# Performance work log

Hardware: AMD Instinct MI355X
Metric: run time of the kernel (lower is better)

Reference implementation:

```python
import jax, jax.numpy as jnp
import numpy as np

N, E, G = 50000, 1600000, 8
IN, H, C = 64, 4, 32
HID = H * C  # 128
L = 3


def setup_inputs() -> dict:
    key = jax.random.key(0)
    ks = jax.random.split(key, 20)
    x = jax.random.normal(ks[0], (N, IN), dtype=jnp.float32)
    edge_index = jax.random.randint(ks[1], (2, E), 0, N, dtype=jnp.int64)
    batch = jnp.sort(jax.random.randint(ks[2], (N,), 0, G, dtype=jnp.int64))
    s = 0.05
    Wp = jax.random.normal(ks[3], (IN, HID), dtype=jnp.float32) * s
    bp = jnp.zeros((HID,), dtype=jnp.float32)
    Wl = jax.random.normal(ks[4], (L, HID, HID), dtype=jnp.float32) * s
    att_src = jax.random.normal(ks[5], (L, H, C), dtype=jnp.float32) * s
    att_dst = jax.random.normal(ks[6], (L, H, C), dtype=jnp.float32) * s
    bconv = jnp.zeros((L, HID), dtype=jnp.float32)
    W1 = jax.random.normal(ks[7], (2 * HID, 256), dtype=jnp.float32) * s
    b1 = jnp.zeros((256,), dtype=jnp.float32)
    W2 = jax.random.normal(ks[8], (256, 128), dtype=jnp.float32) * s
    b2 = jnp.zeros((128,), dtype=jnp.float32)
    W3 = jax.random.normal(ks[9], (128, 1), dtype=jnp.float32) * s
    b3 = jnp.zeros((1,), dtype=jnp.float32)
    return dict(x=x, edge_index=edge_index, batch=batch, Wp=Wp, bp=bp, Wl=Wl,
                att_src=att_src, att_dst=att_dst, bconv=bconv,
                W1=W1, b1=b1, W2=W2, b2=b2, W3=W3, b3=b3)


def _gat_layer(x, src, dst, W, a_src, a_dst, b):
    # PyG GATConv (concat=True, add_self_loops handled by caller via src/dst)
    h = (x @ W).reshape(N, H, C)                      # [N,H,C]
    asrc = jnp.sum(h * a_src, axis=-1)                # [N,H]
    adst = jnp.sum(h * a_dst, axis=-1)                # [N,H]
    e = jax.nn.leaky_relu(asrc[src] + adst[dst], 0.2)  # [E',H]
    m = jax.ops.segment_max(e, dst, num_segments=N)   # scatter-softmax over dst
    e = jnp.exp(e - m[dst])
    z = jax.ops.segment_sum(e, dst, num_segments=N)
    alpha = e / (z[dst] + 1e-16)                      # [E',H]
    out = jax.ops.segment_sum(h[src] * alpha[:, :, None], dst, num_segments=N)
    return out.reshape(N, HID) + b


def reference(x, edge_index, batch, Wp, bp, Wl, att_src, att_dst, bconv,
              W1, b1, W2, b2, W3, b3):
    # add self loops once (PyG default add_self_loops=True)
    loop = jnp.arange(N, dtype=edge_index.dtype)
    src = jnp.concatenate([edge_index[0], loop])
    dst = jnp.concatenate([edge_index[1], loop])

    h = jax.nn.relu(x @ Wp + bp)
    for l in range(L):
        h = jax.nn.relu(_gat_layer(h, src, dst, Wl[l], att_src[l], att_dst[l], bconv[l]))

    cnt = jax.ops.segment_sum(jnp.ones((N,), h.dtype), batch, num_segments=G)
    mean = jax.ops.segment_sum(h, batch, num_segments=G) / jnp.maximum(cnt, 1.0)[:, None]
    mx = jax.ops.segment_max(h, batch, num_segments=G)
    mx = jnp.where(cnt[:, None] > 0, mx, 0.0)
    p = jnp.concatenate([mean, mx], axis=-1)          # [G, 2*HID]

    p = jax.nn.relu(p @ W1 + b1)
    p = jax.nn.relu(p @ W2 + b2)
    return (p @ W3 + b3).squeeze(-1)                  # [G]
```

## Files before the change

### kernel.cpp

```cpp
#include <hip/hip_runtime.h>
#include <math.h>

#define NN 50000
#define GG 8
#define HEADS 4
#define CH 32
#define HID 128
#define NLAYER 3
#define POOL_S 64
#define DEG_CAP 96
#define NBG2 ((NN + 63) / 64)
#define NBS 1024

__device__ float g_h[(size_t)NN * HID];
__device__ __attribute__((aligned(16))) unsigned short g_h2b[(size_t)NN * HID];
__device__ float g_as[(size_t)NN * HEADS];
__device__ float g_ad[(size_t)NN * HEADS];
__device__ int g_cursor[NN];
__device__ __attribute__((aligned(16))) unsigned short g_csr16[(size_t)NN * DEG_CAP];
__device__ int g_starts[GG + 1];
__device__ double g_psum[(size_t)GG * POOL_S * HID];
__device__ float g_pmax[(size_t)GG * POOL_S * HID];

__device__ __forceinline__ float lrelu(float v) { return v > 0.f ? v : 0.2f * v; }

__device__ __forceinline__ float bf2f(unsigned short u) {
    union { unsigned int i; float f; } v;
    v.i = ((unsigned int)u) << 16;
    return v.f;
}
__device__ __forceinline__ unsigned short f2bf(float f) {
    union { float f; unsigned int i; } v;
    v.f = f;
    unsigned int r = v.i + 0x7FFFu + ((v.i >> 16) & 1u);
    return (unsigned short)(r >> 16);
}

__global__ void zero_kernel() {
    int i = blockIdx.x * blockDim.x + threadIdx.x;
    if (i < NN) g_cursor[i] = 0;
}

template <int K, bool ATT, bool RELU, bool SRC_PARAM>
__device__ __forceinline__ void gemm_body(
    const float* __restrict__ Xp, const float* __restrict__ W, const float* __restrict__ bias,
    const float* __restrict__ att_s, const float* __restrict__ att_d, int n, int blk) {
    constexpr int KT = 32;
    constexpr int XS = 68;
    __shared__ float Ws[KT * 128];
    __shared__ float Xs[KT * XS];
    const float* X = SRC_PARAM ? Xp : g_h;
    int tid = threadIdx.x;
    int base = blk * 64;
    int rows = n - base;
    if (rows > 64) rows = 64;
    int cg = tid & 15, rg = tid >> 4;
    int c0 = cg * 8, r0 = rg * 4;
    float acc[4][8];
#pragma unroll
    for (int i = 0; i < 4; i++)
#pragma unroll
        for (int j = 0; j < 8; j++) acc[i][j] = 0.f;

    for (int kb = 0; kb < K; kb += KT) {
        {
            const float4* Wg = (const float4*)(W + (size_t)kb * 128);
            float4* Ws4 = (float4*)Ws;
#pragma unroll
            for (int u = 0; u < 4; u++) Ws4[tid + u * 256] = Wg[tid + u * 256];
        }
#pragma unroll
        for (int u = 0; u < 2; u++) {
            int i = tid + u * 256;
            int r = i >> 3, k4 = i & 7;
            float4 v = {0.f, 0.f, 0.f, 0.f};
            if (r < rows) v = *(const float4*)(X + (size_t)(base + r) * K + kb + k4 * 4);
            Xs[(k4 * 4 + 0) * XS + r] = v.x;
            Xs[(k4 * 4 + 1) * XS + r] = v.y;
            Xs[(k4 * 4 + 2) * XS + r] = v.z;
            Xs[(k4 * 4 + 3) * XS + r] = v.w;
        }
        __syncthreads();
#pragma unroll 8
        for (int k = 0; k < KT; k++) {
            const float4 xa = *(const float4*)&Xs[k * XS + r0];
            const float4 wa = *(const float4*)&Ws[k * 128 + c0];
            const float4 wb = *(const float4*)&Ws[k * 128 + c0 + 4];
            const float xr[4] = {xa.x, xa.y, xa.z, xa.w};
            const float wr[8] = {wa.x, wa.y, wa.z, wa.w, wb.x, wb.y, wb.z, wb.w};
#pragma unroll
            for (int ii = 0; ii < 4; ii++)
#pragma unroll
                for (int jj = 0; jj < 8; jj++) acc[ii][jj] += xr[ii] * wr[jj];
        }
        __syncthreads();
    }

    if constexpr (!ATT) {
        float bv[8];
#pragma unroll
        for (int j = 0; j < 8; j++) bv[j] = bias ? bias[c0 + j] : 0.f;
#pragma unroll
        for (int ii = 0; ii < 4; ii++) {
            int r = r0 + ii;
            if (r < rows) {
                float o[8];
#pragma unroll
                for (int jj = 0; jj < 8; jj++) {
                    o[jj] = acc[ii][jj] + bv[jj];
                    if (RELU) o[jj] = fmaxf(o[jj], 0.f);
                }
                float4 oa = {o[0], o[1], o[2], o[3]};
                float4 ob = {o[4], o[5], o[6], o[7]};
                *(float4*)&g_h[(size_t)(base + r) * 128 + c0] = oa;
                *(float4*)&g_h[(size_t)(base + r) * 128 + c0 + 4] = ob;
            }
        }
    } else {
#pragma unroll
        for (int ii = 0; ii < 4; ii++) {
            int r = r0 + ii;
            if (r < rows) {
                uint4 pk;
                pk.x = (unsigned)f2bf(acc[ii][0]) | ((unsigned)f2bf(acc[ii][1]) << 16);
                pk.y = (unsigned)f2bf(acc[ii][2]) | ((unsigned)f2bf(acc[ii][3]) << 16);
                pk.z = (unsigned)f2bf(acc[ii][4]) | ((unsigned)f2bf(acc[ii][5]) << 16);
                pk.w = (unsigned)f2bf(acc[ii][6]) | ((unsigned)f2bf(acc[ii][7]) << 16);
                *(uint4*)&g_h2b[(size_t)(base + r) * 128 + c0] = pk;
            }
        }
        float avs[8], avd[8];
#pragma unroll
        for (int j = 0; j < 8; j++) { avs[j] = att_s[c0 + j]; avd[j] = att_d[c0 + j]; }
#pragma unroll
        for (int ii = 0; ii < 4; ii++) {
            float ps = 0.f, pd = 0.f;
#pragma unroll
            for (int jj = 0; jj < 8; jj++) { ps += acc[ii][jj] * avs[jj]; pd += acc[ii][jj] * avd[jj]; }
            ps += __shfl_xor(ps, 1); ps += __shfl_xor(ps, 2);
            pd += __shfl_xor(pd, 1); pd += __shfl_xor(pd, 2);
            int r = r0 + ii;
            if ((cg & 3) == 0 && r < rows) {
                g_as[(size_t)(base + r) * 4 + (cg >> 2)] = ps;
                g_ad[(size_t)(base + r) * 4 + (cg >> 2)] = pd;
            }
        }
    }
}

template <int K, bool ATT, bool RELU, bool SRC_PARAM>
__global__ __launch_bounds__(256) void gemm_kernel(
    const float* __restrict__ Xp, const float* __restrict__ W, const float* __restrict__ bias,
    const float* __restrict__ att_s, const float* __restrict__ att_d, int n) {
    gemm_body<K, ATT, RELU, SRC_PARAM>(Xp, W, bias, att_s, att_d, n, blockIdx.x);
}

template <int K, bool ATT, bool RELU, bool SRC_PARAM>
__global__ __launch_bounds__(256) void fat_kernel(
    const float* __restrict__ Xp, const float* __restrict__ W, const float* __restrict__ bias,
    const float* __restrict__ as_, const float* __restrict__ ad_,
    const int* __restrict__ srcv, const int* __restrict__ dstv, int ebeg, int eend) {
    if (blockIdx.x < NBG2) {
        gemm_body<K, ATT, RELU, SRC_PARAM>(Xp, W, bias, as_, ad_, NN, blockIdx.x);
    } else {
        int idx = ebeg + (blockIdx.x - NBG2) * 256 + threadIdx.x;
        int stride = (gridDim.x - NBG2) * 256;
        for (int j = idx; j < eend; j += stride) {
            int d = dstv[j];
            int pos = atomicAdd(&g_cursor[d], 1);
            if (pos < DEG_CAP) g_csr16[(size_t)d * DEG_CAP + pos] = (unsigned short)srcv[j];
        }
    }
}

__global__ __launch_bounds__(256) void gat_layer_kernel(const float* __restrict__ bconv) {
    int wave = threadIdx.x >> 6;
    int lane = threadIdx.x & 63;
    int i = blockIdx.x * 4 + wave;

    int deg = g_cursor[i];
    if (deg > DEG_CAP) deg = DEG_CAP;

    int stream = lane >> 5;
    int sl = lane & 31;
    int hl = sl >> 3;
    int li = sl & 7;
    int c0 = sl * 4;
    int bsel = lane & 56;

    float ad_h = g_ad[(size_t)i * 4 + hl];
    const unsigned short* csr = &g_csr16[(size_t)i * DEG_CAP];

    float4 acc = {0.f, 0.f, 0.f, 0.f};
    float zraw = 0.f;

    int nfull = deg >> 4;
    for (int t = 0; t < nfull; ++t) {
        int j0 = t * 16 + stream * 8;
        uint4 cs = *(const uint4*)(csr + j0);
        int s0 = cs.x & 0xFFFF, s1 = cs.x >> 16;
        int s2 = cs.y & 0xFFFF, s3 = cs.y >> 16;
        int s4 = cs.z & 0xFFFF, s5 = cs.z >> 16;
        int s6 = cs.w & 0xFFFF, s7 = cs.w >> 16;
        ushort4 q0 = *(const ushort4*)&g_h2b[(s0 << 7) + c0];
        ushort4 q1 = *(const ushort4*)&g_h2b[(s1 << 7) + c0];
        ushort4 q2 = *(const ushort4*)&g_h2b[(s2 << 7) + c0];
        ushort4 q3 = *(const ushort4*)&g_h2b[(s3 << 7) + c0];
        ushort4 q4 = *(const ushort4*)&g_h2b[(s4 << 7) + c0];
        ushort4 q5 = *(const ushort4*)&g_h2b[(s5 << 7) + c0];
        ushort4 q6 = *(const ushort4*)&g_h2b[(s6 << 7) + c0];
        ushort4 q7 = *(const ushort4*)&g_h2b[(s7 << 7) + c0];
        unsigned wsel = li < 4 ? (li < 2 ? cs.x : cs.y) : (li < 6 ? cs.z : cs.w);
        int sm = (li & 1) ? (int)(wsel >> 16) : (int)(wsel & 0xFFFF);
        float a = g_as[(sm << 2) + hl];
        float wr = expf(lrelu(a + ad_h));
        zraw += wr;
        float w0 = __shfl(wr, bsel | 0);
        float w1 = __shfl(wr, bsel | 1);
        float w2 = __shfl(wr, bsel | 2);
        float w3 = __shfl(wr, bsel | 3);
        float w4 = __shfl(wr, bsel | 4);
        float w5 = __shfl(wr, bsel | 5);
        float w6 = __shfl(wr, bsel | 6);
        float w7 = __shfl(wr, bsel | 7);
        acc.x += w0 * bf2f(q0.x); acc.y += w0 * bf2f(q0.y); acc.z += w0 * bf2f(q0.z); acc.w += w0 * bf2f(q0.w);
        acc.x += w1 * bf2f(q1.x); acc.y += w1 * bf2f(q1.y); acc.z += w1 * bf2f(q1.z); acc.w += w1 * bf2f(q1.w);
        acc.x += w2 * bf2f(q2.x); acc.y += w2 * bf2f(q2.y); acc.z += w2 * bf2f(q2.z); acc.w += w2 * bf2f(q2.w);
        acc.x += w3 * bf2f(q3.x); acc.y += w3 * bf2f(q3.y); acc.z += w3 * bf2f(q3.z); acc.w += w3 * bf2f(q3.w);
        acc.x += w4 * bf2f(q4.x); acc.y += w4 * bf2f(q4.y); acc.z += w4 * bf2f(q4.z); acc.w += w4 * bf2f(q4.w);
        acc.x += w5 * bf2f(q5.x); acc.y += w5 * bf2f(q5.y); acc.z += w5 * bf2f(q5.z); acc.w += w5 * bf2f(q5.w);
        acc.x += w6 * bf2f(q6.x); acc.y += w6 * bf2f(q6.y); acc.z += w6 * bf2f(q6.z); acc.w += w6 * bf2f(q6.w);
        acc.x += w7 * bf2f(q7.x); acc.y += w7 * bf2f(q7.y); acc.z += w7 * bf2f(q7.z); acc.w += w7 * bf2f(q7.w);
    }

    int tbase = nfull * 16 + stream * 8;
#pragma unroll
    for (int k = 0; k < 8; ++k) {
        if (tbase + k < deg) {
            int s = csr[tbase + k];
            float a = g_as[(s << 2) + hl];
            float wr = expf(lrelu(a + ad_h));
            zraw += wr * 0.125f;
            ushort4 q = *(const ushort4*)&g_h2b[(s << 7) + c0];
            acc.x += wr * bf2f(q.x); acc.y += wr * bf2f(q.y);
            acc.z += wr * bf2f(q.z); acc.w += wr * bf2f(q.w);
        }
    }

    acc.x += __shfl_xor(acc.x, 32);
    acc.y += __shfl_xor(acc.y, 32);
    acc.z += __shfl_xor(acc.z, 32);
    acc.w += __shfl_xor(acc.w, 32);
    zraw += __shfl_xor(zraw, 1);
    zraw += __shfl_xor(zraw, 2);
    zraw += __shfl_xor(zraw, 4);
    zraw += __shfl_xor(zraw, 32);

    if (lane < 32) {
        float as_i = g_as[(i << 2) + hl];
        float sw = expf(lrelu(as_i + ad_h));
        float invz = 1.f / (zraw + sw + 1e-16f);
        ushort4 qs = *(const ushort4*)&g_h2b[(i << 7) + c0];
        float4 bc = *(const float4*)&bconv[c0];
        float4 o;
        o.x = fmaxf((sw * bf2f(qs.x) + acc.x) * invz + bc.x, 0.f);
        o.y = fmaxf((sw * bf2f(qs.y) + acc.y) * invz + bc.y, 0.f);
        o.z = fmaxf((sw * bf2f(qs.z) + acc.z) * invz + bc.z, 0.f);
        o.w = fmaxf((sw * bf2f(qs.w) + acc.w) * invz + bc.w, 0.f);
        *(float4*)&g_h[(size_t)i * 128 + c0] = o;
    }
}

__global__ void bounds_kernel(const int* __restrict__ batch) {
    int t = threadIdx.x;
    if (t > GG) return;
    int lo = 0, hi = NN;
    while (lo < hi) {
        int mid = (lo + hi) >> 1;
        if (batch[mid] < t) lo = mid + 1; else hi = mid;
    }
    g_starts[t] = lo;
}

__global__ void pool1_kernel() {
    int g = blockIdx.x / POOL_S, s = blockIdx.x % POOL_S;
    int n0 = g_starts[g], n1 = g_starts[g + 1];
    long long cnt = n1 - n0;
    int a = n0 + (int)(cnt * s / POOL_S);
    int b = n0 + (int)(cnt * (s + 1) / POOL_S);
    int c = threadIdx.x;
    double sum = 0.0;
    float mx = -INFINITY;
    for (int nn = a; nn < b; nn++) {
        float v = g_h[(size_t)nn * 128 + c];
        sum += v;
        mx = fmaxf(mx, v);
    }
    g_psum[(size_t)blockIdx.x * 128 + c] = sum;
    g_pmax[(size_t)blockIdx.x * 128 + c] = mx;
}

__global__ __launch_bounds__(256) void head_kernel(
    const float* __restrict__ W1, const float* __restrict__ b1,
    const float* __restrict__ W2, const float* __restrict__ b2,
    const float* __restrict__ W3, const float* __restrict__ b3,
    float* __restrict__ outv) {
    __shared__ float p[256];
    __shared__ float r1[256];
    __shared__ float r2[128];
    int g = blockIdx.x, t = threadIdx.x;
    int cnt = g_starts[g + 1] - g_starts[g];
    if (t < 128) {
        double s = 0.0;
        for (int q = 0; q < POOL_S; q++) s += g_psum[(size_t)(g * POOL_S + q) * 128 + t];
        double dcnt = cnt > 0 ? (double)cnt : 1.0;
        p[t] = (float)(s / dcnt);
    } else {
        int c = t - 128;
        float mx = -INFINITY;
        for (int q = 0; q < POOL_S; q++) mx = fmaxf(mx, g_pmax[(size_t)(g * POOL_S + q) * 128 + c]);
        p[t] = cnt > 0 ? mx : 0.f;
    }
    __syncthreads();
    float acc = b1[t];
    for (int k = 0; k < 256; k++) acc += p[k] * W1[k * 256 + t];
    r1[t] = fmaxf(acc, 0.f);
    __syncthreads();
    if (t < 128) {
        float a2 = b2[t];
        for (int k = 0; k < 256; k++) a2 += r1[k] * W2[k * 128 + t];
        r2[t] = fmaxf(a2, 0.f);
    }
    __syncthreads();
    if (t < 64) {
        float a3 = r2[t] * W3[t] + r2[t + 64] * W3[t + 64];
#pragma unroll
        for (int d = 32; d >= 1; d >>= 1) a3 += __shfl_down(a3, d);
        if (t == 0) outv[g] = a3 + b3[0];
    }
}

extern "C" void kernel_launch(void* const* d_in, const int* in_sizes, int n_in,
                              void* d_out, int out_size, void* d_ws, size_t ws_size,
                              hipStream_t stream) {
    const float* x = (const float*)d_in[0];
    const int* eidx = (const int*)d_in[1];
    const int* batch = (const int*)d_in[2];
    const float* Wp = (const float*)d_in[3];
    const float* bp = (const float*)d_in[4];
    const float* Wl = (const float*)d_in[5];
    const float* att_src = (const float*)d_in[6];
    const float* att_dst = (const float*)d_in[7];
    const float* bconv = (const float*)d_in[8];
    const float* W1 = (const float*)d_in[9];
    const float* b1 = (const float*)d_in[10];
    const float* W2 = (const float*)d_in[11];
    const float* b2 = (const float*)d_in[12];
    const float* W3 = (const float*)d_in[13];
    const float* b3 = (const float*)d_in[14];
    float* out = (float*)d_out;
    int E = in_sizes[1] / 2;
    int Emid = E / 2;

    zero_kernel<<<(NN + 255) / 256, 256, 0, stream>>>();

    fat_kernel<64, false, true, true><<<NBG2 + NBS, 256, 0, stream>>>(
        x, Wp, bp, nullptr, nullptr, eidx, eidx + E, 0, Emid);

    fat_kernel<128, true, false, false><<<NBG2 + NBS, 256, 0, stream>>>(
        nullptr, Wl, nullptr, att_src, att_dst, eidx, eidx + E, Emid, E);

    gat_layer_kernel<<<NN / 4, 256, 0, stream>>>(bconv);

    for (int l = 1; l < NLAYER; l++) {
        gemm_kernel<128, true, false, false><<<NBG2, 256, 0, stream>>>(
            nullptr, Wl + (size_t)l * HID * HID, nullptr,
            att_src + (size_t)l * HEADS * CH, att_dst + (size_t)l * HEADS * CH, NN);
        gat_layer_kernel<<<NN / 4, 256, 0, stream>>>(bconv + (size_t)l * HID);
    }

    bounds_kernel<<<1, 64, 0, stream>>>(batch);
    pool1_kernel<<<GG * POOL_S, 128, 0, stream>>>();
    head_kernel<<<GG, 256, 0, stream>>>(W1, b1, W2, b2, W3, b3, out);
}
```

Before: 533.4 us.

## Use split-bf16 MFMA for GAT layer projections with hi/lo activation storage

Replaces the FP32 FMA tiled GEMM for the per-layer 128x128 projection with MFMA 16x16x32 bf16 instructions. Activations and weights are each split into bf16 high and low parts, and three products are accumulated to keep close to FP32 accuracy. The producing kernels now write hi/lo bf16 activations instead of fp32, and a weight-transpose prep kernel is added. This trades FP32 ALU work for matrix-core work, but adds extra conversion work and the weight-prep launch, and the operands are loaded straight from global memory without LDS staging.

```diff
diff --git a/kernel.cpp b/kernel.cpp
--- a/kernel.cpp
+++ b/kernel.cpp
@@ -12,8 +12,15 @@
 #define NBG2 ((NN + 63) / 64)
 #define NBS 1024
 
+typedef __attribute__((ext_vector_type(8))) short bf16x8;
+typedef __attribute__((ext_vector_type(4))) float f32x4;
+
 __device__ float g_h[(size_t)NN * HID];
 __device__ __attribute__((aligned(16))) unsigned short g_h2b[(size_t)NN * HID];
+__device__ __attribute__((aligned(16))) unsigned short g_xhi[(size_t)NN * HID];
+__device__ __attribute__((aligned(16))) unsigned short g_xlo[(size_t)NN * HID];
+__device__ __attribute__((aligned(16))) unsigned short g_wthi[(size_t)NLAYER * HID * HID];
+__device__ __attribute__((aligned(16))) unsigned short g_wtlo[(size_t)NLAYER * HID * HID];
 __device__ float g_as[(size_t)NN * HEADS];
 __device__ float g_ad[(size_t)NN * HEADS];
 __device__ int g_cursor[NN];
@@ -41,18 +48,30 @@
     if (i < NN) g_cursor[i] = 0;
 }
 
-template <int K, bool ATT, bool RELU, bool SRC_PARAM>
-__device__ __forceinline__ void gemm_body(
+__global__ void wprep_kernel(const float* __restrict__ Wl) {
+    int idx = blockIdx.x * 256 + threadIdx.x;
+    if (idx >= NLAYER * HID * HID) return;
+    int lay = idx / (HID * HID);
+    int rem = idx - lay * HID * HID;
+    int n = rem >> 7, k = rem & 127;
+    float v = Wl[(size_t)lay * HID * HID + (size_t)k * HID + n];
+    unsigned short h = f2bf(v);
+    float r = v - bf2f(h);
+    g_wthi[idx] = h;
+    g_wtlo[idx] = f2bf(r);
+}
+
+template <int K>
+__device__ __forceinline__ void proj_body(
     const float* __restrict__ Xp, const float* __restrict__ W, const float* __restrict__ bias,
-    const float* __restrict__ att_s, const float* __restrict__ att_d, int n, int blk) {
+    int blk) {
     constexpr int KT = 32;
     constexpr int XS = 68;
     __shared__ float Ws[KT * 128];
     __shared__ float Xs[KT * XS];
-    const float* X = SRC_PARAM ? Xp : g_h;
     int tid = threadIdx.x;
     int base = blk * 64;
-    int rows = n - base;
+    int rows = NN - base;
     if (rows > 64) rows = 64;
     int cg = tid & 15, rg = tid >> 4;
     int c0 = cg * 8, r0 = rg * 4;
@@ -74,7 +93,7 @@
             int i = tid + u * 256;
             int r = i >> 3, k4 = i & 7;
             float4 v = {0.f, 0.f, 0.f, 0.f};
-            if (r < rows) v = *(const float4*)(X + (size_t)(base + r) * K + kb + k4 * 4);
+            if (r < rows) v = *(const float4*)(Xp + (size_t)(base + r) * K + kb + k4 * 4);
             Xs[(k4 * 4 + 0) * XS + r] = v.x;
             Xs[(k4 * 4 + 1) * XS + r] = v.y;
             Xs[(k4 * 4 + 2) * XS + r] = v.z;
@@ -96,83 +115,137 @@
         __syncthreads();
     }
 
-    if constexpr (!ATT) {
-        float bv[8];
-#pragma unroll
-        for (int j = 0; j < 8; j++) bv[j] = bias ? bias[c0 + j] : 0.f;
-#pragma unroll
-        for (int ii = 0; ii < 4; ii++) {
-            int r = r0 + ii;
-            if (r < rows) {
-                float o[8];
-#pragma unroll
-                for (int jj = 0; jj < 8; jj++) {
-                    o[jj] = acc[ii][jj] + bv[jj];
-                    if (RELU) o[jj] = fmaxf(o[jj], 0.f);
-                }
-                float4 oa = {o[0], o[1], o[2], o[3]};
-                float4 ob = {o[4], o[5], o[6], o[7]};
-                *(float4*)&g_h[(size_t)(base + r) * 128 + c0] = oa;
-                *(float4*)&g_h[(size_t)(base + r) * 128 + c0 + 4] = ob;
-            }
-        }
-    } else {
-#pragma unroll
-        for (int ii = 0; ii < 4; ii++) {
-            int r = r0 + ii;
-            if (r < rows) {
-                uint4 pk;
-                pk.x = (unsigned)f2bf(acc[ii][0]) | ((unsigned)f2bf(acc[ii][1]) << 16);
-                pk.y = (unsigned)f2bf(acc[ii][2]) | ((unsigned)f2bf(acc[ii][3]) << 16);
-                pk.z = (unsigned)f2bf(acc[ii][4]) | ((unsigned)f2bf(acc[ii][5]) << 16);
-                pk.w = (unsigned)f2bf(acc[ii][6]) | ((unsigned)f2bf(acc[ii][7]) << 16);
-                *(uint4*)&g_h2b[(size_t)(base + r) * 128 + c0] = pk;
-            }
-        }
-        float avs[8], avd[8];
-#pragma unroll
-        for (int j = 0; j < 8; j++) { avs[j] = att_s[c0 + j]; avd[j] = att_d[c0 + j]; }
-#pragma unroll
-        for (int ii = 0; ii < 4; ii++) {
-            float ps = 0.f, pd = 0.f;
-#pragma unroll
-            for (int jj = 0; jj < 8; jj++) { ps += acc[ii][jj] * avs[jj]; pd += acc[ii][jj] * avd[jj]; }
-            ps += __shfl_xor(ps, 1); ps += __shfl_xor(ps, 2);
-            pd += __shfl_xor(pd, 1); pd += __shfl_xor(pd, 2);
-            int r = r0 + ii;
-            if ((cg & 3) == 0 && r < rows) {
-                g_as[(size_t)(base + r) * 4 + (cg >> 2)] = ps;
-                g_ad[(size_t)(base + r) * 4 + (cg >> 2)] = pd;
-            }
-        }
-    }
-}
-
-template <int K, bool ATT, bool RELU, bool SRC_PARAM>
-__global__ __launch_bounds__(256) void gemm_kernel(
+    float bv[8];
+#pragma unroll
+    for (int j = 0; j < 8; j++) bv[j] = bias[c0 + j];
+#pragma unroll
+    for (int ii = 0; ii < 4; ii++) {
+        int r = r0 + ii;
+        if (r < rows) {
+            ushort4 h0, l0, h1, l1;
+            float o[8];
+#pragma unroll
+            for (int jj = 0; jj < 8; jj++) o[jj] = fmaxf(acc[ii][jj] + bv[jj], 0.f);
+            h0.x = f2bf(o[0]); h0.y = f2bf(o[1]); h0.z = f2bf(o[2]); h0.w = f2bf(o[3]);
+            h1.x = f2bf(o[4]); h1.y = f2bf(o[5]); h1.z = f2bf(o[6]); h1.w = f2bf(o[7]);
+            l0.x = f2bf(o[0] - bf2f(h0.x)); l0.y = f2bf(o[1] - bf2f(h0.y));
+            l0.z = f2bf(o[2] - bf2f(h0.z)); l0.w = f2bf(o[3] - bf2f(h0.w));
+            l1.x = f2bf(o[4] - bf2f(h1.x)); l1.y = f2bf(o[5] - bf2f(h1.y));
+            l1.z = f2bf(o[6] - bf2f(h1.z)); l1.w = f2bf(o[7] - bf2f(h1.w));
+            size_t off = (size_t)(base + r) * 128 + c0;
+            *(ushort4*)&g_xhi[off] = h0;
+            *(ushort4*)&g_xhi[off + 4] = h1;
+            *(ushort4*)&g_xlo[off] = l0;
+            *(ushort4*)&g_xlo[off + 4] = l1;
+        }
+    }
+}
+
+__device__ __forceinline__ void mfma_att_body(
+    const float* __restrict__ att_s, const float* __restrict__ att_d,
+    int lay, int blk) {
+    __shared__ float Ysh[64][HID];
+    int tid = threadIdx.x;
+    int w = tid >> 6, l = tid & 63;
+    int base = blk * 64;
+    int rows = NN - base;
+    if (rows > 64) rows = 64;
+    int ar = l & 15, kg = l >> 4;
+    int arow = base + w * 16 + ar;
+    if (arow >= NN) arow = NN - 1;
+    const unsigned short* xh = g_xhi + (size_t)arow * HID + kg * 8;
+    const unsigned short* xl = g_xlo + (size_t)arow * HID + kg * 8;
+    const unsigned short* wh = g_wthi + (size_t)lay * HID * HID + (size_t)ar * HID + kg * 8;
+    const unsigned short* wl = g_wtlo + (size_t)lay * HID * HID + (size_t)ar * HID + kg * 8;
+
+    f32x4 acc[8];
+#pragma unroll
+    for (int ct = 0; ct < 8; ct++) acc[ct] = (f32x4){0.f, 0.f, 0.f, 0.f};
+
+#pragma unroll
+    for (int ks = 0; ks < 4; ks++) {
+        bf16x8 ah = *(const bf16x8*)(xh + ks * 32);
+        bf16x8 al = *(const bf16x8*)(xl + ks * 32);
+#pragma unroll
+        for (int ct = 0; ct < 8; ct++) {
+            bf16x8 bh = *(const bf16x8*)(wh + ct * 16 * HID + ks * 32);
+            bf16x8 bl = *(const bf16x8*)(wl + ct * 16 * HID + ks * 32);
+            acc[ct] = __builtin_amdgcn_mfma_f32_16x16x32_bf16(ah, bh, acc[ct], 0, 0, 0);
+            acc[ct] = __builtin_amdgcn_mfma_f32_16x16x32_bf16(al, bh, acc[ct], 0, 0, 0);
+            acc[ct] = __builtin_amdgcn_mfma_f32_16x16x32_bf16(ah, bl, acc[ct], 0, 0, 0);
+        }
+    }
+
+#pragma unroll
+    for (int ct = 0; ct < 8; ct++)
+#pragma unroll
+        for (int j = 0; j < 4; j++)
+            Ysh[w * 16 + kg * 4 + j][ct * 16 + ar] = acc[ct][j];
+    __syncthreads();
+
+    int cg = tid & 15, rg = tid >> 4;
+    int c0 = cg * 8, r0 = rg * 4;
+    float avs[8], avd[8];
+#pragma unroll
+    for (int j = 0; j < 8; j++) { avs[j] = att_s[c0 + j]; avd[j] = att_d[c0 + j]; }
+#pragma unroll
+    for (int ii = 0; ii < 4; ii++) {
+        int r = r0 + ii;
+        float o[8];
+#pragma unroll
+        for (int jj = 0; jj < 8; jj++) o[jj] = Ysh[r][c0 + jj];
+        if (r < rows) {
+            uint4 pk;
+            pk.x = (unsigned)f2bf(o[0]) | ((unsigned)f2bf(o[1]) << 16);
+            pk.y = (unsigned)f2bf(o[2]) | ((unsigned)f2bf(o[3]) << 16);
+            pk.z = (unsigned)f2bf(o[4]) | ((unsigned)f2bf(o[5]) << 16);
+            pk.w = (unsigned)f2bf(o[6]) | ((unsigned)f2bf(o[7]) << 16);
+            *(uint4*)&g_h2b[(size_t)(base + r) * 128 + c0] = pk;
+        }
+        float ps = 0.f, pd = 0.f;
+#pragma unroll
+        for (int jj = 0; jj < 8; jj++) { ps += o[jj] * avs[jj]; pd += o[jj] * avd[jj]; }
+        ps += __shfl_xor(ps, 1); ps += __shfl_xor(ps, 2);
+        pd += __shfl_xor(pd, 1); pd += __shfl_xor(pd, 2);
+        if ((cg & 3) == 0 && r < rows) {
+            g_as[(size_t)(base + r) * 4 + (cg >> 2)] = ps;
+            g_ad[(size_t)(base + r) * 4 + (cg >> 2)] = pd;
+        }
+    }
+}
+
+__device__ __forceinline__ void scatter_body(
+    const int* __restrict__ srcv, const int* __restrict__ dstv,
+    int ebeg, int eend, int blk, int nblk) {
+    int idx = ebeg + blk * 256 + threadIdx.x;
+    int stride = nblk * 256;
+    for (int j = idx; j < eend; j += stride) {
+        int d = dstv[j];
+        int pos = atomicAdd(&g_cursor[d], 1);
+        if (pos < DEG_CAP) g_csr16[(size_t)d * DEG_CAP + pos] = (unsigned short)srcv[j];
+    }
+}
+
+__global__ __launch_bounds__(256) void fat1_kernel(
     const float* __restrict__ Xp, const float* __restrict__ W, const float* __restrict__ bias,
-    const float* __restrict__ att_s, const float* __restrict__ att_d, int n) {
-    gemm_body<K, ATT, RELU, SRC_PARAM>(Xp, W, bias, att_s, att_d, n, blockIdx.x);
-}
-
-template <int K, bool ATT, bool RELU, bool SRC_PARAM>
-__global__ __launch_bounds__(256) void fat_kernel(
-    const float* __restrict__ Xp, const float* __restrict__ W, const float* __restrict__ bias,
-    const float* __restrict__ as_, const float* __restrict__ ad_,
     const int* __restrict__ srcv, const int* __restrict__ dstv, int ebeg, int eend) {
-    if (blockIdx.x < NBG2) {
-        gemm_body<K, ATT, RELU, SRC_PARAM>(Xp, W, bias, as_, ad_, NN, blockIdx.x);
-    } else {
-        int idx = ebeg + (blockIdx.x - NBG2) * 256 + threadIdx.x;
-        int stride = (gridDim.x - NBG2) * 256;
-        for (int j = idx; j < eend; j += stride) {
-            int d = dstv[j];
-            int pos = atomicAdd(&g_cursor[d], 1);
-            if (pos < DEG_CAP) g_csr16[(size_t)d * DEG_CAP + pos] = (unsigned short)srcv[j];
-        }
-    }
-}
-
+    if (blockIdx.x < NBG2) proj_body<64>(Xp, W, bias, blockIdx.x);
+    else scatter_body(srcv, dstv, ebeg, eend, blockIdx.x - NBG2, gridDim.x - NBG2);
+}
+
+__global__ __launch_bounds__(256, 2) void fat2_kernel(
+    const float* __restrict__ att_s, const float* __restrict__ att_d,
+    const int* __restrict__ srcv, const int* __restrict__ dstv, int ebeg, int eend) {
+    if (blockIdx.x < NBG2) mfma_att_body(att_s, att_d, 0, blockIdx.x);
+    else scatter_body(srcv, dstv, ebeg, eend, blockIdx.x - NBG2, gridDim.x - NBG2);
+}
+
+__global__ __launch_bounds__(256, 2) void att_gemm_kernel(
+    const float* __restrict__ att_s, const float* __restrict__ att_d, int lay) {
+    mfma_att_body(att_s, att_d, lay, blockIdx.x);
+}
+
+template <bool LAST>
 __global__ __launch_bounds__(256) void gat_layer_kernel(const float* __restrict__ bconv) {
     int wave = threadIdx.x >> 6;
     int lane = threadIdx.x & 63;
@@ -267,7 +340,16 @@
         o.y = fmaxf((sw * bf2f(qs.y) + acc.y) * invz + bc.y, 0.f);
         o.z = fmaxf((sw * bf2f(qs.z) + acc.z) * invz + bc.z, 0.f);
         o.w = fmaxf((sw * bf2f(qs.w) + acc.w) * invz + bc.w, 0.f);
-        *(float4*)&g_h[(size_t)i * 128 + c0] = o;
+        if (LAST) {
+            *(float4*)&g_h[(size_t)i * 128 + c0] = o;
+        } else {
+            ushort4 hh, ll;
+            hh.x = f2bf(o.x); hh.y = f2bf(o.y); hh.z = f2bf(o.z); hh.w = f2bf(o.w);
+            ll.x = f2bf(o.x - bf2f(hh.x)); ll.y = f2bf(o.y - bf2f(hh.y));
+            ll.z = f2bf(o.z - bf2f(hh.z)); ll.w = f2bf(o.w - bf2f(hh.w));
+            *(ushort4*)&g_xhi[(size_t)i * 128 + c0] = hh;
+            *(ushort4*)&g_xlo[(size_t)i * 128 + c0] = ll;
+        }
     }
 }
 
@@ -363,21 +445,21 @@
     int Emid = E / 2;
 
     zero_kernel<<<(NN + 255) / 256, 256, 0, stream>>>();
-
-    fat_kernel<64, false, true, true><<<NBG2 + NBS, 256, 0, stream>>>(
-        x, Wp, bp, nullptr, nullptr, eidx, eidx + E, 0, Emid);
-
-    fat_kernel<128, true, false, false><<<NBG2 + NBS, 256, 0, stream>>>(
-        nullptr, Wl, nullptr, att_src, att_dst, eidx, eidx + E, Emid, E);
-
-    gat_layer_kernel<<<NN / 4, 256, 0, stream>>>(bconv);
-
-    for (int l = 1; l < NLAYER; l++) {
-        gemm_kernel<128, true, false, false><<<NBG2, 256, 0, stream>>>(
-            nullptr, Wl + (size_t)l * HID * HID, nullptr,
-            att_src + (size_t)l * HEADS * CH, att_dst + (size_t)l * HEADS * CH, NN);
-        gat_layer_kernel<<<NN / 4, 256, 0, stream>>>(bconv + (size_t)l * HID);
-    }
+    wprep_kernel<<<(NLAYER * HID * HID + 255) / 256, 256, 0, stream>>>(Wl);
+
+    fat1_kernel<<<NBG2 + NBS, 256, 0, stream>>>(x, Wp, bp, eidx, eidx + E, 0, Emid);
+
+    fat2_kernel<<<NBG2 + NBS, 256, 0, stream>>>(att_src, att_dst, eidx, eidx + E, Emid, E);
+
+    gat_layer_kernel<false><<<NN / 4, 256, 0, stream>>>(bconv);
+
+    att_gemm_kernel<<<NBG2, 256, 0, stream>>>(
+        att_src + (size_t)1 * HEADS * CH, att_dst + (size_t)1 * HEADS * CH, 1);
+    gat_layer_kernel<false><<<NN / 4, 256, 0, stream>>>(bconv + (size_t)1 * HID);
+
+    att_gemm_kernel<<<NBG2, 256, 0, stream>>>(
+        att_src + (size_t)2 * HEADS * CH, att_dst + (size_t)2 * HEADS * CH, 2);
+    gat_layer_kernel<true><<<NN / 4, 256, 0, stream>>>(bconv + (size_t)2 * HID);
 
     bounds_kernel<<<1, 64, 0, stream>>>(batch);
     pool1_kernel<<<GG * POOL_S, 128, 0, stream>>>();
```

Result: no change. 541.4 us (+1.5%).
